# Performance work log

Hardware: AMD Instinct MI355X
Metric: run time of the kernel (lower is better)

The kernel has to match this reference:

```python
import jax, jax.numpy as jnp
import numpy as np


def setup_inputs() -> dict:
    key = jax.random.key(0)
    k1, k2 = jax.random.split(key)
    N, K, C = 2, 32, 32
    h, w = 64, 64
    H, W = 1024, 1024
    grid = jax.random.normal(k1, (N, K, C, h, w), dtype=jnp.float32)
    guidemap = jax.random.normal(k2, (N, C, H, W), dtype=jnp.float32)
    return {"grid": grid, "guidemap": guidemap}


def reference(grid, guidemap):
    N, C, H, W = guidemap.shape
    h, w = grid.shape[3], grid.shape[4]
    f1, f2 = H // h, W // w
    # F.unfold with kernel==stride (non-overlapping blocks):
    # [N,C,H,W] -> [N,C,f1*f2,h,w] with kernel elements row-major within a block.
    g = guidemap.reshape(N, C, h, f1, w, f2)
    g = g.transpose(0, 1, 3, 5, 2, 4).reshape(N, C, f1 * f2, h, w)
    # Per-location small contraction over channels C.
    out = jnp.einsum('ikjmn,ijlmn->iklmn', grid, g)  # [N,K,f1*f2,h,w]
    # F.fold with kernel==stride (non-overlapping scatter, no overlap-add):
    out = out.reshape(N, -1, f1, f2, h, w)
    out = out.transpose(0, 1, 4, 2, 5, 3).reshape(N, -1, H, W)
    return out
```

## Files before the change

### kernel.cpp

```cpp
#include <hip/hip_runtime.h>


namespace {
constexpr int NIMG = 2;
constexpr int K = 32;
constexpr int C = 32;
constexpr int HB = 64, WB = 64;
constexpr int F1 = 16, F2 = 16;
constexpr int H = 1024, W = 1024;
constexpr int HW = H * W;
}

__global__ __launch_bounds__(512, 4) void gridup_kernel(
    const float* __restrict__ grd,
    const float* __restrict__ gm,
    float* __restrict__ out)
{
    __shared__ float4 sG4[C][64];
    __shared__ float4 sM4[C][K / 4];

    const int b   = blockIdx.x;
    const int n   = b >> 12;
    const int rem = b & 4095;
    const int by  = rem >> 6;
    const int bx  = rem & 63;
    const int t   = threadIdx.x;

    {
        const float* gbase = gm + (size_t)n * C * HW + (by * F1) * W + bx * F2;
        #pragma unroll
        for (int i = 0; i < 4; ++i) {
            const int e   = t + 512 * i;
            const int c   = e >> 6;
            const int l   = e & 63;
            const int r   = l >> 2;
            const int col = (l & 3) << 2;
            sG4[c][l] = *reinterpret_cast<const float4*>(
                gbase + (size_t)c * HW + r * W + col);
        }
    }
    {
        const float* mb = grd + (size_t)n * (K * C * HB * WB) + by * WB + bx;
        float* sMf = reinterpret_cast<float*>(&sM4[0][0]);
        #pragma unroll
        for (int i = 0; i < 2; ++i) {
            const int e = t + 512 * i;
            const int k = e & 31;
            const int c = e >> 5;
            sMf[e] = mb[(size_t)(k * C + c) * (HB * WB)];
        }
    }
    __syncthreads();

    const int kg = t >> 6;
    const int l  = t & 63;

    float acc[4][4] = {};
    #pragma unroll
    for (int c = 0; c < C; ++c) {
        const float4 g = sG4[c][l];
        const float4 m = sM4[c][kg];
        const float gv[4] = {g.x, g.y, g.z, g.w};
        const float mv[4] = {m.x, m.y, m.z, m.w};
        #pragma unroll
        for (int dk = 0; dk < 4; ++dk) {
            #pragma unroll
            for (int p = 0; p < 4; ++p) {
                acc[dk][p] += mv[dk] * gv[p];
            }
        }
    }

    const int r   = l >> 2;
    const int col = (l & 3) << 2;
    float* ob = out + ((size_t)n * K + kg * 4) * HW + (by * F1 + r) * W + bx * F2 + col;
    #pragma unroll
    for (int dk = 0; dk < 4; ++dk) {
        const float4 v = {acc[dk][0], acc[dk][1], acc[dk][2], acc[dk][3]};
        *reinterpret_cast<float4*>(ob + (size_t)dk * HW) = v;
    }
}

extern "C" void kernel_launch(void* const* d_in, const int* in_sizes, int n_in,
                              void* d_out, int out_size, void* d_ws, size_t ws_size,
                              hipStream_t stream) {
    const float* grd = (const float*)d_in[0];
    const float* gm  = (const float*)d_in[1];
    float* out = (float*)d_out;

    const int nblocks = NIMG * HB * WB;
    gridup_kernel<<<nblocks, 512, 0, stream>>>(grd, gm, out);
}
```

Measured before the change: 190.2 us.

## Restructure kernel: two tiles per block, per-thread all-K accumulators, direct guide loads

Each block now handles two 16x16 tiles with 256 threads. Each thread owns 2 pixels and all 32 output channels, reading the guide map straight from global memory as float2 with software double-buffering instead of staging it in LDS. The per-tile 32x32 weight matrices are loaded into LDS via global_load_lds, and block indices are swizzled across groups of 8. The design trades more registers (64 accumulators) and narrower float2 stores for fewer LDS round trips and better reuse of the weights per thread.

```diff
diff --git a/kernel.cpp b/kernel.cpp
--- a/kernel.cpp
+++ b/kernel.cpp
@@ -2,82 +2,97 @@
 
 
 namespace {
-constexpr int NIMG = 2;
-constexpr int K = 32;
-constexpr int C = 32;
-constexpr int HB = 64, WB = 64;
-constexpr int F1 = 16, F2 = 16;
-constexpr int H = 1024, W = 1024;
-constexpr int HW = H * W;
+constexpr int K = 32, C = 32;
+constexpr int W = 1024;
+constexpr int HW = 1024 * 1024;
+constexpr size_t GRDN = (size_t)K * C * 64 * 64;
 }
 
-__global__ __launch_bounds__(512, 4) void gridup_kernel(
+__device__ __forceinline__ void gl_lds4(const float* src, float* dst) {
+    __builtin_amdgcn_global_load_lds(
+        (const __attribute__((address_space(1))) void*)src,
+        (__attribute__((address_space(3))) void*)dst, 4, 0, 0);
+}
+
+__global__ __launch_bounds__(256, 4) void gridup_kernel(
     const float* __restrict__ grd,
     const float* __restrict__ gm,
     float* __restrict__ out)
 {
-    __shared__ float4 sG4[C][64];
-    __shared__ float4 sM4[C][K / 4];
+    __shared__ float sM[2][C][K];
 
-    const int b   = blockIdx.x;
-    const int n   = b >> 12;
-    const int rem = b & 4095;
-    const int by  = rem >> 6;
-    const int bx  = rem & 63;
-    const int t   = threadIdx.x;
+    int wg = blockIdx.x;
+    wg = (wg & 7) * 512 + (wg >> 3);
+    const int t = threadIdx.x;
+    const int g0 = wg * 2;
 
-    {
-        const float* gbase = gm + (size_t)n * C * HW + (by * F1) * W + bx * F2;
-        #pragma unroll
-        for (int i = 0; i < 4; ++i) {
-            const int e   = t + 512 * i;
-            const int c   = e >> 6;
-            const int l   = e & 63;
-            const int r   = l >> 2;
-            const int col = (l & 3) << 2;
-            sG4[c][l] = *reinterpret_cast<const float4*>(
-                gbase + (size_t)c * HW + r * W + col);
-        }
-    }
-    {
-        const float* mb = grd + (size_t)n * (K * C * HB * WB) + by * WB + bx;
-        float* sMf = reinterpret_cast<float*>(&sM4[0][0]);
-        #pragma unroll
-        for (int i = 0; i < 2; ++i) {
-            const int e = t + 512 * i;
-            const int k = e & 31;
-            const int c = e >> 5;
-            sMf[e] = mb[(size_t)(k * C + c) * (HB * WB)];
-        }
+    #pragma unroll
+    for (int i = 0; i < 8; ++i) {
+        const int e  = i * 256 + t;
+        const int t2 = e >> 10;
+        const int c  = (e >> 5) & 31;
+        const int k  = e & 31;
+        const int gt2 = g0 + t2;
+        const int n2  = gt2 >> 12;
+        const int rr2 = gt2 & 4095;
+        const int by2 = rr2 >> 6;
+        const int bx2 = rr2 & 63;
+        gl_lds4(grd + (size_t)n2 * GRDN + (size_t)(k * 32 + c) * 4096 + by2 * 64 + bx2,
+                &sM[0][0][0] + e);
     }
     __syncthreads();
 
-    const int kg = t >> 6;
-    const int l  = t & 63;
+    const int tl = t >> 7;
+    const int gt = g0 + tl;
+    const int n  = gt >> 12;
+    const int rr = gt & 4095;
+    const int by = rr >> 6;
+    const int bx = rr & 63;
 
-    float acc[4][4] = {};
+    const float* M = &sM[tl][0][0];
+    const int p   = (t & 127) * 2;
+    const int row = p >> 4;
+    const int col = p & 15;
+    const size_t pix = (size_t)(by * 16 + row) * W + bx * 16 + col;
+    const float* gb = gm + (size_t)n * C * HW + pix;
+    float*       ob = out + (size_t)n * K * HW + pix;
+
+    float acc[32][2] = {};
+    float2 gc[4], gn[4];
     #pragma unroll
-    for (int c = 0; c < C; ++c) {
-        const float4 g = sG4[c][l];
-        const float4 m = sM4[c][kg];
-        const float gv[4] = {g.x, g.y, g.z, g.w};
-        const float mv[4] = {m.x, m.y, m.z, m.w};
+    for (int j = 0; j < 4; ++j)
+        gc[j] = *reinterpret_cast<const float2*>(gb + (size_t)j * HW);
+
+    for (int cb = 0; cb < 8; ++cb) {
+        if (cb < 7) {
+            #pragma unroll
+            for (int j = 0; j < 4; ++j)
+                gn[j] = *reinterpret_cast<const float2*>(
+                    gb + (size_t)((cb + 1) * 4 + j) * HW);
+        }
         #pragma unroll
-        for (int dk = 0; dk < 4; ++dk) {
+        for (int j = 0; j < 4; ++j) {
+            const int c = cb * 4 + j;
+            const float2 g = gc[j];
             #pragma unroll
-            for (int p = 0; p < 4; ++p) {
-                acc[dk][p] += mv[dk] * gv[p];
+            for (int kq = 0; kq < 8; ++kq) {
+                const float4 m = *reinterpret_cast<const float4*>(M + c * 32 + kq * 4);
+                acc[kq * 4 + 0][0] += m.x * g.x;  acc[kq * 4 + 0][1] += m.x * g.y;
+                acc[kq * 4 + 1][0] += m.y * g.x;  acc[kq * 4 + 1][1] += m.y * g.y;
+                acc[kq * 4 + 2][0] += m.z * g.x;  acc[kq * 4 + 2][1] += m.z * g.y;
+                acc[kq * 4 + 3][0] += m.w * g.x;  acc[kq * 4 + 3][1] += m.w * g.y;
             }
+        }
+        if (cb < 7) {
+            #pragma unroll
+            for (int j = 0; j < 4; ++j) gc[j] = gn[j];
         }
     }
 
-    const int r   = l >> 2;
-    const int col = (l & 3) << 2;
-    float* ob = out + ((size_t)n * K + kg * 4) * HW + (by * F1 + r) * W + bx * F2 + col;
     #pragma unroll
-    for (int dk = 0; dk < 4; ++dk) {
-        const float4 v = {acc[dk][0], acc[dk][1], acc[dk][2], acc[dk][3]};
-        *reinterpret_cast<float4*>(ob + (size_t)dk * HW) = v;
+    for (int k = 0; k < 32; ++k) {
+        const float2 v = {acc[k][0], acc[k][1]};
+        *reinterpret_cast<float2*>(ob + (size_t)k * HW) = v;
     }
 }
 
@@ -88,6 +103,5 @@
     const float* gm  = (const float*)d_in[1];
     float* out = (float*)d_out;
 
-    const int nblocks = NIMG * HB * WB;
-    gridup_kernel<<<nblocks, 512, 0, stream>>>(grd, gm, out);
+    gridup_kernel<<<4096, 256, 0, stream>>>(grd, gm, out);
 }
```

Measured after the change: 165.2 us. 1.15x faster.
